# Kernel optimization log

Hardware: AMD Instinct MI355X
Metric: run time of the kernel (lower is better)

## Reference

```python
import jax, jax.numpy as jnp
import numpy as np

PH = PW = 7          # pooled output size
SR = 2               # sampling_ratio: SR x SR samples per bin
SCALES = (0.25, 0.125, 0.0625, 0.03125)  # FPN strides 4,8,16,32
K = 512              # number of ROIs
B = 2                # batch (images)
IMG = 800.0


def _coords(start, bsize, P):
    # sample coords for P bins, SR samples per bin: start + p*bin + (i+0.5)*bin/SR
    j = jnp.arange(P * SR, dtype=start.dtype)
    return (start[:, None]
            + (j // SR)[None, :] * bsize[:, None]
            + ((j % SR) + 0.5)[None, :] * (bsize[:, None] / SR))  # [K, P*SR]


def _roi_align_level(feat, rois, scale):
    # feat: [B, C, H, W] ; rois: [K, 5] (batch_idx, x1, y1, x2, y2 in image coords)
    Bf, C, H, W = feat.shape
    b = rois[:, 0].astype(jnp.int32)
    x1 = rois[:, 1] * scale
    y1 = rois[:, 2] * scale
    x2 = rois[:, 3] * scale
    y2 = rois[:, 4] * scale
    roi_w = jnp.maximum(x2 - x1, 1.0)   # legacy (aligned=False) ROIAlign
    roi_h = jnp.maximum(y2 - y1, 1.0)
    ys = _coords(y1, roi_h / PH, PH)    # [K, Sy]
    xs = _coords(x1, roi_w / PW, PW)    # [K, Sx]
    y = ys[:, :, None]                  # [K, Sy, 1]
    x = xs[:, None, :]                  # [K, 1, Sx]
    valid = (y > -1.0) & (y < H) & (x > -1.0) & (x < W)  # [K, Sy, Sx]
    yc = jnp.clip(y, 0.0, None)
    xc = jnp.clip(x, 0.0, None)
    yl = jnp.minimum(yc.astype(jnp.int32), H - 1)
    xl = jnp.minimum(xc.astype(jnp.int32), W - 1)
    yh = jnp.minimum(yl + 1, H - 1)
    xh = jnp.minimum(xl + 1, W - 1)
    ly = jnp.where(yl >= H - 1, 0.0, yc - yl)
    lx = jnp.where(xl >= W - 1, 0.0, xc - xl)
    hy, hx = 1.0 - ly, 1.0 - lx
    feat_flat = feat.reshape(Bf, C, H * W)
    Sy, Sx = PH * SR, PW * SR
    acc = jnp.zeros((rois.shape[0], C, Sy, Sx), feat.dtype)
    corners = ((yl, xl, hy * hx), (yl, xh, hy * lx),
               (yh, xl, ly * hx), (yh, xh, ly * lx))
    for yy, xx, w in corners:  # fixed 4-corner loop (not a data-dim loop)
        idx = jnp.broadcast_to(yy * W + xx, (rois.shape[0], Sy, Sx))
        vals = jax.vmap(lambda bi, ii: jnp.take(feat_flat, bi, axis=0)[:, ii])(b, idx)
        acc = acc + vals * jnp.broadcast_to(w, idx.shape)[:, None, :, :]
    acc = jnp.where(valid[:, None, :, :], acc, 0.0)
    # average SRxSR samples within each 7x7 bin
    return acc.reshape(rois.shape[0], C, PH, SR, PW, SR).mean(axis=(3, 5))


def setup_inputs() -> dict:
    key = jax.random.key(0)
    ks = jax.random.split(key, 10)
    input_0 = jax.random.normal(ks[0], (B, 256, 200, 200), jnp.float32)
    input_1 = jax.random.normal(ks[1], (B, 256, 100, 100), jnp.float32)
    input_2 = jax.random.normal(ks[2], (B, 256, 50, 50), jnp.float32)
    input_3 = jax.random.normal(ks[3], (B, 256, 25, 25), jnp.float32)
    bidx = jax.random.randint(ks[4], (K,), 0, B).astype(jnp.float32)
    x1 = jax.random.uniform(ks[5], (K,)) * (IMG - 64.0)
    y1 = jax.random.uniform(ks[6], (K,)) * (IMG - 64.0)
    bw = 32.0 + jax.random.uniform(ks[7], (K,)) * 200.0
    bh = 32.0 + jax.random.uniform(ks[8], (K,)) * 200.0
    rois = jnp.stack([bidx, x1, y1,
                      jnp.minimum(x1 + bw, IMG),
                      jnp.minimum(y1 + bh, IMG)], axis=1).astype(jnp.float32)
    level = jax.random.randint(ks[9], (K,), 0, 4).astype(jnp.int32)
    rois_counts = jnp.array([K // 2, K - K // 2], jnp.int32)  # unused (all ROIs valid)
    return {"input_0": input_0, "input_1": input_1, "input_2": input_2,
            "input_3": input_3, "rois": rois, "rois_counts": rois_counts,
            "level": level}


def reference(input_0, input_1, input_2, input_3, rois, rois_counts, level):
    feats = (input_0, input_1, input_2, input_3)
    lvl = level.astype(jnp.int32)
    out = jnp.zeros((rois.shape[0], input_0.shape[1], PH, PW), input_0.dtype)
    for i, (f, s) in enumerate(zip(feats, SCALES)):
        o = _roi_align_level(f, rois, s)
        out = out + jnp.where((lvl == i)[:, None, None, None], o, 0.0)
    return out
```

## Files before the change

### kernel.cpp

```cpp
#include <hip/hip_runtime.h>


#define NUM_CH 256
#define CPT    4
#define CGRP   64

typedef float floatx2 __attribute__((ext_vector_type(2)));
typedef float floatx4 __attribute__((ext_vector_type(4)));

__device__ __forceinline__ float ext4(floatx4 v, int i) {
    float r = (i == 1) ? v.y : v.x;
    r = (i == 2) ? v.z : r;
    r = (i == 3) ? v.w : r;
    return r;
}

__global__ __launch_bounds__(256) void roi_align_kernel(
    const float* __restrict__ f0,
    const float* __restrict__ f1,
    const float* __restrict__ f2,
    const float* __restrict__ f3,
    const float* __restrict__ rois_f,
    const int* __restrict__ level,
    float* __restrict__ out,
    int total)
{
    int u = blockIdx.x * blockDim.x + threadIdx.x;
    if (u >= total) return;

    int p  = u % 49;
    int t  = u / 49;
    int c2 = t % CGRP;
    int k  = t / CGRP;
    int ph = p / 7;
    int pw = p % 7;

    int lvl = level[k];
    const float* f;
    int H, W; float scale;
    if (lvl == 0)      { f = f0; H = 200; W = 200; scale = 0.25f;    }
    else if (lvl == 1) { f = f1; H = 100; W = 100; scale = 0.125f;   }
    else if (lvl == 2) { f = f2; H = 50;  W = 50;  scale = 0.0625f;  }
    else               { f = f3; H = 25;  W = 25;  scale = 0.03125f; }

    const float* rf = rois_f + (size_t)k * 5;
    float r0 = rf[0];
    float x1 = rf[1] * scale, y1 = rf[2] * scale;
    float x2 = rf[3] * scale, y2 = rf[4] * scale;
    int bi = (int)r0;
    bi = (bi < 0) ? 0 : ((bi > 1) ? 1 : bi);

    float bh = fmaxf(y2 - y1, 1.0f) * (1.0f / 7.0f);
    float bw = fmaxf(x2 - x1, 1.0f) * (1.0f / 7.0f);

    const size_t plane = (size_t)(H * W);
    const float* base  = f + ((size_t)bi * NUM_CH + c2) * plane;
    const size_t cstr  = (size_t)CGRP * plane;

    int   rA[2], rB[2];
    float lyv[2], hyv[2], vy[2];
    #pragma unroll
    for (int sy = 0; sy < 2; ++sy) {
        float y = y1 + (float)ph * bh + ((float)sy + 0.5f) * (bh * 0.5f);
        bool valid = (y > -1.0f) && (y < (float)H);
        float yc = fmaxf(y, 0.0f);
        int yl = min((int)yc, H - 1);
        int yh = min(yl + 1, H - 1);
        float ly = (yl >= H - 1) ? 0.0f : (yc - (float)yl);
        rA[sy] = yl * W;
        rB[sy] = yh * W;
        lyv[sy] = ly; hyv[sy] = 1.0f - ly;
        vy[sy] = valid ? 0.25f : 0.0f;
    }
    int   xlv[2], xhv[2];
    float lxv[2], hxv[2], vx[2];
    #pragma unroll
    for (int sx = 0; sx < 2; ++sx) {
        float x = x1 + (float)pw * bw + ((float)sx + 0.5f) * (bw * 0.5f);
        bool valid = (x > -1.0f) && (x < (float)W);
        float xc = fmaxf(x, 0.0f);
        int xl = min((int)xc, W - 1);
        float lx = (xl >= W - 1) ? 0.0f : (xc - (float)xl);
        xlv[sx] = xl;
        xhv[sx] = min(xl + 1, W - 1);
        lxv[sx] = lx; hxv[sx] = 1.0f - lx;
        vx[sx] = valid ? 1.0f : 0.0f;
    }

    float acc[CPT];
    #pragma unroll
    for (int j = 0; j < CPT; ++j) acc[j] = 0.0f;

    if (bw <= 3.98f) {
        int xq = min(xlv[0], W - 4);
        int i0l = min(max(xlv[0] - xq, 0), 3);
        int i0h = min(max(xhv[0] - xq, 0), 3);
        int i1l = min(max(xlv[1] - xq, 0), 3);
        int i1h = min(max(xhv[1] - xq, 0), 3);

        #pragma unroll
        for (int sy = 0; sy < 2; ++sy) {
            floatx4 LA[CPT], LB[CPT];
            #pragma unroll
            for (int j = 0; j < CPT; ++j) {
                const float* bj = base + (size_t)j * cstr;
                LA[j] = *(const floatx4*)(bj + rA[sy] + xq);
                LB[j] = *(const floatx4*)(bj + rB[sy] + xq);
            }
            #pragma unroll
            for (int sx = 0; sx < 2; ++sx) {
                int il = sx ? i1l : i0l;
                int ih = sx ? i1h : i0h;
                float vs  = vy[sy] * vx[sx];
                float w00 = hyv[sy] * hxv[sx] * vs;
                float w01 = hyv[sy] * lxv[sx] * vs;
                float w10 = lyv[sy] * hxv[sx] * vs;
                float w11 = lyv[sy] * lxv[sx] * vs;
                #pragma unroll
                for (int j = 0; j < CPT; ++j) {
                    acc[j] += w00 * ext4(LA[j], il) + w01 * ext4(LA[j], ih)
                            + w10 * ext4(LB[j], il) + w11 * ext4(LB[j], ih);
                }
            }
        }
    } else {
        int   xb[2];
        float sel[2];
        #pragma unroll
        for (int sx = 0; sx < 2; ++sx) {
            int xq = min(xlv[sx], W - 2);
            xb[sx]  = xq;
            sel[sx] = (xlv[sx] > xq) ? 1.0f : 0.0f;
        }
        #pragma unroll
        for (int sy = 0; sy < 2; ++sy) {
            floatx2 va[CPT][2], vb[CPT][2];
            #pragma unroll
            for (int sx = 0; sx < 2; ++sx) {
                #pragma unroll
                for (int j = 0; j < CPT; ++j) {
                    const float* bj = base + (size_t)j * cstr;
                    va[j][sx] = *(const floatx2*)(bj + rA[sy] + xb[sx]);
                    vb[j][sx] = *(const floatx2*)(bj + rB[sy] + xb[sx]);
                }
            }
            #pragma unroll
            for (int sx = 0; sx < 2; ++sx) {
                float vs  = vy[sy] * vx[sx];
                float w00 = hyv[sy] * hxv[sx] * vs;
                float w01 = hyv[sy] * lxv[sx] * vs;
                float w10 = lyv[sy] * hxv[sx] * vs;
                float w11 = lyv[sy] * lxv[sx] * vs;
                float s0  = sel[sx];
                #pragma unroll
                for (int j = 0; j < CPT; ++j) {
                    float v00 = va[j][sx].x + s0 * (va[j][sx].y - va[j][sx].x);
                    float v10 = vb[j][sx].x + s0 * (vb[j][sx].y - vb[j][sx].x);
                    acc[j] += w00 * v00 + w01 * va[j][sx].y
                            + w10 * v10 + w11 * vb[j][sx].y;
                }
            }
        }
    }

    size_t ob = ((size_t)k * NUM_CH + c2) * 49 + p;
    #pragma unroll
    for (int j = 0; j < CPT; ++j)
        out[ob + (size_t)j * (CGRP * 49)] = acc[j];
}

extern "C" void kernel_launch(void* const* d_in, const int* in_sizes, int n_in,
                              void* d_out, int out_size, void* d_ws, size_t ws_size,
                              hipStream_t stream) {
    const float* f0   = (const float*)d_in[0];
    const float* f1   = (const float*)d_in[1];
    const float* f2   = (const float*)d_in[2];
    const float* f3   = (const float*)d_in[3];
    const float* rois = (const float*)d_in[4];
    const int* level = (const int*)d_in[6];
    float* out = (float*)d_out;

    int total = out_size / CPT;
    int threads = 256;
    int blocks = (total + threads - 1) / threads;
    roi_align_kernel<<<blocks, threads, 0, stream>>>(f0, f1, f2, f3, rois, level, out, total);
}
```

Before: 189.0 us.

## Map one wavefront per ROI-channel group with XCD-aware block remapping

Each 64-lane wavefront now handles a single (ROI, channel-group) pair, with lanes 0-48 covering the 49 output bins and lanes 49-63 left idle. ROI and channel indices are made wave-uniform through readfirstlane, so the level, ROI and coordinate setup runs on scalar registers and control flow does not diverge. Block IDs are remapped so consecutive logical blocks land on the same XCD, and work is ordered ROI-fastest within a channel group, which aims to improve L2 locality for feature loads. The cost is roughly 23% idle lanes and more blocks to launch.

```diff
diff --git a/kernel.cpp b/kernel.cpp
--- a/kernel.cpp
+++ b/kernel.cpp
@@ -23,15 +23,26 @@
     const float* __restrict__ rois_f,
     const int* __restrict__ level,
     float* __restrict__ out,
-    int total)
+    int K,
+    int NW)
 {
-    int u = blockIdx.x * blockDim.x + threadIdx.x;
-    if (u >= total) return;
+    int nb  = gridDim.x;
+    int q   = nb >> 3, r = nb & 7;
+    int xcd = blockIdx.x & 7;
+    int idx = blockIdx.x >> 3;
+    int l   = xcd * q + min(xcd, r) + idx;
 
-    int p  = u % 49;
-    int t  = u / 49;
-    int c2 = t % CGRP;
-    int k  = t / CGRP;
+    int wid = l * 4 + (int)(threadIdx.x >> 6);
+    if (wid >= NW) return;
+    int lane = threadIdx.x & 63;
+    if (lane >= 49) return;
+
+    int k  = wid % K;
+    int c2 = wid / K;
+    k  = __builtin_amdgcn_readfirstlane(k);
+    c2 = __builtin_amdgcn_readfirstlane(c2);
+
+    int p  = lane;
     int ph = p / 7;
     int pw = p % 7;
 
@@ -180,8 +191,9 @@
     const int* level = (const int*)d_in[6];
     float* out = (float*)d_out;
 
-    int total = out_size / CPT;
+    int K  = out_size / (NUM_CH * 49);
+    int NW = K * CGRP;
     int threads = 256;
-    int blocks = (total + threads - 1) / threads;
-    roi_align_kernel<<<blocks, threads, 0, stream>>>(f0, f1, f2, f3, rois, level, out, total);
+    int blocks  = (NW + 3) / 4;
+    roi_align_kernel<<<blocks, threads, 0, stream>>>(f0, f1, f2, f3, rois, level, out, K, NW);
 }
```

Result: faster. 184.5 us (median of 2 runs) (-2.4%).
